# Performance work log

Measured on AMD Instinct MI355X. Metric: run time of the kernel, lower is better.

The kernel has to match this reference:

```python
import jax, jax.numpy as jnp
import numpy as np
from jax.scipy.special import logsumexp

N_ITERS = 20


def setup_inputs() -> dict:
    key = jax.random.key(0)
    k1, _ = jax.random.split(key)
    cost_matrix = jax.random.uniform(k1, (64, 1024, 1024), dtype=jnp.float32)
    epsilon = jnp.ones((1,), dtype=jnp.float32)
    return {"cost_matrix": cost_matrix, "epsilon": epsilon}


def reference(cost_matrix, epsilon):
    # log-space Sinkhorn: alternate row / column normalization in log domain
    log_alpha = -cost_matrix / epsilon  # (B, N, N)

    def step(la, _):
        la = la - logsumexp(la, axis=-1, keepdims=True)  # row normalize
        la = la - logsumexp(la, axis=-2, keepdims=True)  # col normalize
        return la, None

    log_alpha, _ = jax.lax.scan(step, log_alpha, None, length=N_ITERS)
    return jnp.exp(log_alpha)
```

## Files before the change

### kernel.cpp

```cpp
#include <hip/hip_runtime.h>
#include <hip/hip_fp16.h>


#define BATCH 64
#define N 1024
#define NITERS 20
#define ROWS_PER_BLOCK 64
#define BLOCKS_PER_BATCH (N / ROWS_PER_BLOCK)
#define THREADS 256
#define NU2 (N / 4)

union H2U { __half2 h; unsigned u; };

__device__ __forceinline__ uint2 f4_to_h4(float4 f) {
    H2U a, b;
    a.h = __float22half2_rn(make_float2(f.x, f.y));
    b.h = __float22half2_rn(make_float2(f.z, f.w));
    uint2 r; r.x = a.u; r.y = b.u;
    return r;
}

__device__ __forceinline__ float4 h4_to_f4(uint2 r) {
    H2U a, b;
    a.u = r.x; b.u = r.y;
    float2 fa = __half22float2(a.h);
    float2 fb = __half22float2(b.h);
    return make_float4(fa.x, fa.y, fb.x, fb.y);
}


__global__ __launch_bounds__(THREADS) void sk_zero(float* __restrict__ csum_all) {
    const int i = blockIdx.x * THREADS + threadIdx.x;
    csum_all[i] = 0.0f;
}

__global__ __launch_bounds__(THREADS) void sk_build(
        const float* __restrict__ C, const float* __restrict__ eps,
        uint2* __restrict__ K, float* __restrict__ u,
        float* __restrict__ csum_out) {
    __shared__ float lds[2][4][8];
    const int t = threadIdx.x;
    const int b = blockIdx.y;
    const int row0 = blockIdx.x * ROWS_PER_BLOCK;
    const int lane = t & 63, wid = t >> 6;
    const float nie = -1.0f / eps[0];

    const float4* __restrict__ Cp = (const float4*)(C + ((size_t)b * N + row0) * N) + t;
    uint2* __restrict__ Kp = K + ((size_t)b * N + row0) * NU2 + t;

    float4 colacc = make_float4(0.f, 0.f, 0.f, 0.f);
    float4 cur[8];
    #pragma unroll
    for (int r = 0; r < 8; ++r) cur[r] = Cp[r * 256];

    for (int chunk = 0; chunk < 8; ++chunk) {
        float4 nxt[8];
        if (chunk < 7) {
            #pragma unroll
            for (int r = 0; r < 8; ++r) nxt[r] = Cp[(chunk * 8 + 8 + r) * 256];
        }
        float4 k[8]; float s[8];
        #pragma unroll
        for (int r = 0; r < 8; ++r) {
            k[r].x = __expf(cur[r].x * nie);
            k[r].y = __expf(cur[r].y * nie);
            k[r].z = __expf(cur[r].z * nie);
            k[r].w = __expf(cur[r].w * nie);
            s[r] = (k[r].x + k[r].y) + (k[r].z + k[r].w);
            Kp[(chunk * 8 + r) * NU2] = f4_to_h4(k[r]);
        }
        #pragma unroll
        for (int off = 32; off; off >>= 1)
            #pragma unroll
            for (int r = 0; r < 8; ++r) s[r] += __shfl_xor(s[r], off, 64);
        const int p = chunk & 1;
        if (lane == 0) {
            #pragma unroll
            for (int r = 0; r < 8; ++r) lds[p][wid][r] = s[r];
        }
        __syncthreads();
        float ui[8];
        #pragma unroll
        for (int r = 0; r < 8; ++r)
            ui[r] = 1.0f / (((lds[p][0][r] + lds[p][1][r]) + (lds[p][2][r] + lds[p][3][r])));
        if (t < 8)
            u[b * N + row0 + chunk * 8 + t] =
                1.0f / ((lds[p][0][t] + lds[p][1][t]) + (lds[p][2][t] + lds[p][3][t]));
        #pragma unroll
        for (int r = 0; r < 8; ++r) {
            colacc.x += k[r].x * ui[r];
            colacc.y += k[r].y * ui[r];
            colacc.z += k[r].z * ui[r];
            colacc.w += k[r].w * ui[r];
        }
        #pragma unroll
        for (int r = 0; r < 8; ++r) cur[r] = nxt[r];
    }
    float* cs = csum_out + b * N + 4 * t;
    atomicAdd(cs + 0, colacc.x);
    atomicAdd(cs + 1, colacc.y);
    atomicAdd(cs + 2, colacc.z);
    atomicAdd(cs + 3, colacc.w);
}

__global__ __launch_bounds__(THREADS) void sk_iter(
        const uint2* __restrict__ K, const float* __restrict__ csum_in,
        float* __restrict__ u, float* __restrict__ csum_out) {
    __shared__ float lds[2][4][8];
    const int t = threadIdx.x;
    const int b = blockIdx.y;
    const int row0 = blockIdx.x * ROWS_PER_BLOCK;
    const int lane = t & 63, wid = t >> 6;

    const float4 ci = ((const float4*)(csum_in + b * N))[t];
    const float4 vv = make_float4(1.0f / ci.x, 1.0f / ci.y, 1.0f / ci.z, 1.0f / ci.w);
    const uint2* __restrict__ Kp = K + ((size_t)b * N + row0) * NU2 + t;

    float4 colacc = make_float4(0.f, 0.f, 0.f, 0.f);
    uint2 cur[8];
    #pragma unroll
    for (int r = 0; r < 8; ++r) cur[r] = Kp[r * NU2];

    for (int chunk = 0; chunk < 8; ++chunk) {
        uint2 nxt[8];
        if (chunk < 7) {
            #pragma unroll
            for (int r = 0; r < 8; ++r) nxt[r] = Kp[(chunk * 8 + 8 + r) * NU2];
        }
        float4 k[8]; float s[8];
        #pragma unroll
        for (int r = 0; r < 8; ++r) {
            k[r] = h4_to_f4(cur[r]);
            s[r] = (k[r].x * vv.x + k[r].y * vv.y) + (k[r].z * vv.z + k[r].w * vv.w);
        }
        #pragma unroll
        for (int off = 32; off; off >>= 1)
            #pragma unroll
            for (int r = 0; r < 8; ++r) s[r] += __shfl_xor(s[r], off, 64);
        const int p = chunk & 1;
        if (lane == 0) {
            #pragma unroll
            for (int r = 0; r < 8; ++r) lds[p][wid][r] = s[r];
        }
        __syncthreads();
        float ui[8];
        #pragma unroll
        for (int r = 0; r < 8; ++r)
            ui[r] = 1.0f / (((lds[p][0][r] + lds[p][1][r]) + (lds[p][2][r] + lds[p][3][r])));
        if (t < 8)
            u[b * N + row0 + chunk * 8 + t] =
                1.0f / ((lds[p][0][t] + lds[p][1][t]) + (lds[p][2][t] + lds[p][3][t]));
        #pragma unroll
        for (int r = 0; r < 8; ++r) {
            colacc.x += k[r].x * ui[r];
            colacc.y += k[r].y * ui[r];
            colacc.z += k[r].z * ui[r];
            colacc.w += k[r].w * ui[r];
        }
        #pragma unroll
        for (int r = 0; r < 8; ++r) cur[r] = nxt[r];
    }
    float* cs = csum_out + b * N + 4 * t;
    atomicAdd(cs + 0, colacc.x);
    atomicAdd(cs + 1, colacc.y);
    atomicAdd(cs + 2, colacc.z);
    atomicAdd(cs + 3, colacc.w);
}

__global__ __launch_bounds__(THREADS) void sk_final(
        const uint2* __restrict__ K, const float* __restrict__ u,
        const float* __restrict__ csum_last, float* __restrict__ out) {
    const int t = threadIdx.x;
    const int row = blockIdx.x;
    const int b = blockIdx.y;
    const float ui = u[b * N + row];
    const float4 ci = ((const float4*)(csum_last + b * N))[t];
    const float4 vv = make_float4(1.0f / ci.x, 1.0f / ci.y, 1.0f / ci.z, 1.0f / ci.w);
    const size_t base = (size_t)b * N + row;
    float4 k = h4_to_f4((K + base * NU2)[t]);
    float4 o;
    o.x = k.x * ui * vv.x;
    o.y = k.y * ui * vv.y;
    o.z = k.z * ui * vv.z;
    o.w = k.w * ui * vv.w;
    ((float4*)(out + base * N))[t] = o;
}


__device__ __forceinline__ float block_reduce_broadcast(float val, float* lds) {
    #pragma unroll
    for (int off = 32; off > 0; off >>= 1)
        val += __shfl_xor(val, off, 64);
    const int lane = threadIdx.x & 63;
    const int wid  = threadIdx.x >> 6;
    if (lane == 0) lds[wid] = val;
    __syncthreads();
    float total = lds[0] + lds[1] + lds[2] + lds[3];
    __syncthreads();
    return total;
}

__global__ __launch_bounds__(THREADS) void sink_init(float* __restrict__ v,
                                                     float* __restrict__ colsum) {
    const int i = blockIdx.x * THREADS + threadIdx.x;
    v[i] = 1.0f;
    colsum[i] = 0.0f;
}

__global__ __launch_bounds__(THREADS) void sink_iter(
        const float* __restrict__ C, const float* __restrict__ eps,
        const float* __restrict__ v, float* __restrict__ u,
        float* __restrict__ colsum) {
    __shared__ float lds[4];
    const int t = threadIdx.x;
    const int b = blockIdx.y;
    const int row0 = blockIdx.x * ROWS_PER_BLOCK;
    const float neg_inv_eps = -1.0f / eps[0];

    const float4 vv = ((const float4*)(v + b * N))[t];
    const float4* __restrict__ Cp = (const float4*)(C + ((size_t)b * N + row0) * N);

    float4 colacc = make_float4(0.f, 0.f, 0.f, 0.f);
    float4 cur = Cp[t];
    for (int i = 0; i < ROWS_PER_BLOCK; ++i) {
        float4 nxt = cur;
        if (i + 1 < ROWS_PER_BLOCK)
            nxt = Cp[(size_t)(i + 1) * (N / 4) + t];

        float4 k;
        k.x = __expf(cur.x * neg_inv_eps);
        k.y = __expf(cur.y * neg_inv_eps);
        k.z = __expf(cur.z * neg_inv_eps);
        k.w = __expf(cur.w * neg_inv_eps);

        float s = k.x * vv.x + k.y * vv.y + k.z * vv.z + k.w * vv.w;
        float S = block_reduce_broadcast(s, lds);
        float ui = 1.0f / S;
        if (t == 0) u[b * N + row0 + i] = ui;

        colacc.x += k.x * ui;
        colacc.y += k.y * ui;
        colacc.z += k.z * ui;
        colacc.w += k.w * ui;
        cur = nxt;
    }

    float* cs = colsum + b * N + 4 * t;
    atomicAdd(cs + 0, colacc.x);
    atomicAdd(cs + 1, colacc.y);
    atomicAdd(cs + 2, colacc.z);
    atomicAdd(cs + 3, colacc.w);
}

__global__ __launch_bounds__(THREADS) void sink_fix(float* __restrict__ v,
                                                    float* __restrict__ colsum) {
    const int i = blockIdx.x * THREADS + threadIdx.x;
    v[i] = 1.0f / colsum[i];
    colsum[i] = 0.0f;
}

__global__ __launch_bounds__(THREADS) void sink_final(
        const float* __restrict__ C, const float* __restrict__ eps,
        const float* __restrict__ u, const float* __restrict__ v,
        float* __restrict__ out) {
    const int t = threadIdx.x;
    const int row = blockIdx.x;
    const int b = blockIdx.y;
    const float neg_inv_eps = -1.0f / eps[0];
    const float ui = u[b * N + row];
    const float4 vv = ((const float4*)(v + b * N))[t];
    const size_t base = ((size_t)b * N + row) * N;
    float4 c = ((const float4*)(C + base))[t];
    float4 o;
    o.x = __expf(c.x * neg_inv_eps) * ui * vv.x;
    o.y = __expf(c.y * neg_inv_eps) * ui * vv.y;
    o.z = __expf(c.z * neg_inv_eps) * ui * vv.z;
    o.w = __expf(c.w * neg_inv_eps) * ui * vv.w;
    ((float4*)(out + base))[t] = o;
}


extern "C" void kernel_launch(void* const* d_in, const int* in_sizes, int n_in,
                              void* d_out, int out_size, void* d_ws, size_t ws_size,
                              hipStream_t stream) {
    const float* C   = (const float*)d_in[0];
    const float* eps = (const float*)d_in[1];
    float* out = (float*)d_out;

    const size_t k_bytes  = (size_t)BATCH * N * N * 2;
    const size_t uv_elems = (size_t)BATCH * N;
    const size_t needed   = k_bytes + uv_elems * 4 * (1 + NITERS);

    if (ws_size >= needed) {
        uint2* K      = (uint2*)d_ws;
        float* u      = (float*)((char*)d_ws + k_bytes);
        float* csum   = u + uv_elems;

        sk_zero<<<dim3(NITERS * uv_elems / THREADS), dim3(THREADS), 0, stream>>>(csum);
        sk_build<<<dim3(BLOCKS_PER_BATCH, BATCH), dim3(THREADS), 0, stream>>>(
            C, eps, K, u, csum);
        for (int it = 2; it <= NITERS; ++it) {
            sk_iter<<<dim3(BLOCKS_PER_BATCH, BATCH), dim3(THREADS), 0, stream>>>(
                K, csum + (size_t)(it - 2) * uv_elems, u,
                csum + (size_t)(it - 1) * uv_elems);
        }
        sk_final<<<dim3(N, BATCH), dim3(THREADS), 0, stream>>>(
            K, u, csum + (size_t)(NITERS - 1) * uv_elems, out);
    } else {
        float* u      = (float*)d_ws;
        float* v      = u + uv_elems;
        float* colsum = v + uv_elems;
        sink_init<<<dim3(BATCH * N / THREADS), dim3(THREADS), 0, stream>>>(v, colsum);
        for (int it = 0; it < NITERS; ++it) {
            sink_iter<<<dim3(BLOCKS_PER_BATCH, BATCH), dim3(THREADS), 0, stream>>>(
                C, eps, v, u, colsum);
            sink_fix<<<dim3(BATCH * N / THREADS), dim3(THREADS), 0, stream>>>(v, colsum);
        }
        sink_final<<<dim3(N, BATCH), dim3(THREADS), 0, stream>>>(C, eps, u, v, out);
    }
}
```

Measured before the change: 1.115 ms.

## Give each wavefront whole rows to drop per-chunk block barriers

The build and iteration kernels are restructured so each 64-lane wavefront owns 16 full rows, with every lane holding 16 contiguous columns loaded as 16-byte vectors. Row sums then need only a wave shuffle reduction, which removes the per-chunk LDS exchange and __syncthreads. Column partial sums from the four waves are combined once through shared memory before the global atomics. In exchange each thread keeps 16 column accumulators, which raises register use, and there is less memory-level parallelism per iteration (two 16-byte loads in flight per thread instead of eight 8-byte loads).

Measured after the change: 1.090 ms. 2.2% less time.

```diff
diff --git a/kernel.cpp b/kernel.cpp
--- a/kernel.cpp
+++ b/kernel.cpp
@@ -9,6 +9,7 @@
 #define BLOCKS_PER_BATCH (N / ROWS_PER_BLOCK)
 #define THREADS 256
 #define NU2 (N / 4)
+#define NU4 (N / 8)
 
 union H2U { __half2 h; unsigned u; };
 
@@ -28,6 +29,25 @@
     return make_float4(fa.x, fa.y, fb.x, fb.y);
 }
 
+__device__ __forceinline__ void h8_unpack(uint4 r, float* f) {
+    H2U a, b, c, d;
+    a.u = r.x; b.u = r.y; c.u = r.z; d.u = r.w;
+    float2 fa = __half22float2(a.h), fb = __half22float2(b.h);
+    float2 fc = __half22float2(c.h), fd = __half22float2(d.h);
+    f[0] = fa.x; f[1] = fa.y; f[2] = fb.x; f[3] = fb.y;
+    f[4] = fc.x; f[5] = fc.y; f[6] = fd.x; f[7] = fd.y;
+}
+
+__device__ __forceinline__ uint4 h8_pack(const float* f) {
+    H2U a, b, c, d;
+    a.h = __float22half2_rn(make_float2(f[0], f[1]));
+    b.h = __float22half2_rn(make_float2(f[2], f[3]));
+    c.h = __float22half2_rn(make_float2(f[4], f[5]));
+    d.h = __float22half2_rn(make_float2(f[6], f[7]));
+    uint4 r; r.x = a.u; r.y = b.u; r.z = c.u; r.w = d.u;
+    return r;
+}
+
 
 __global__ __launch_bounds__(THREADS) void sk_zero(float* __restrict__ csum_all) {
     const int i = blockIdx.x * THREADS + threadIdx.x;
@@ -36,135 +56,145 @@
 
 __global__ __launch_bounds__(THREADS) void sk_build(
         const float* __restrict__ C, const float* __restrict__ eps,
-        uint2* __restrict__ K, float* __restrict__ u,
+        uint4* __restrict__ K, float* __restrict__ u,
         float* __restrict__ csum_out) {
-    __shared__ float lds[2][4][8];
-    const int t = threadIdx.x;
-    const int b = blockIdx.y;
-    const int row0 = blockIdx.x * ROWS_PER_BLOCK;
-    const int lane = t & 63, wid = t >> 6;
+    __shared__ float4 smc[4][N / 4];
+    const int t = threadIdx.x;
+    const int lane = t & 63, w = t >> 6;
+    const int b = blockIdx.y;
+    const int row0 = blockIdx.x * ROWS_PER_BLOCK + w * 16;
     const float nie = -1.0f / eps[0];
 
-    const float4* __restrict__ Cp = (const float4*)(C + ((size_t)b * N + row0) * N) + t;
-    uint2* __restrict__ Kp = K + ((size_t)b * N + row0) * NU2 + t;
-
-    float4 colacc = make_float4(0.f, 0.f, 0.f, 0.f);
-    float4 cur[8];
-    #pragma unroll
-    for (int r = 0; r < 8; ++r) cur[r] = Cp[r * 256];
-
-    for (int chunk = 0; chunk < 8; ++chunk) {
-        float4 nxt[8];
-        if (chunk < 7) {
+    const float4* __restrict__ Cp =
+        (const float4*)(C + ((size_t)b * N + row0) * N) + lane * 4;
+    uint4* __restrict__ Kp = K + ((size_t)b * N + row0) * NU4 + lane * 2;
+
+    float colacc[16];
+    #pragma unroll
+    for (int q = 0; q < 16; ++q) colacc[q] = 0.0f;
+
+    float4 cur[4];
+    #pragma unroll
+    for (int q = 0; q < 4; ++q) cur[q] = Cp[q];
+
+    for (int i = 0; i < 16; ++i) {
+        float4 nxt[4];
+        if (i < 15) {
             #pragma unroll
-            for (int r = 0; r < 8; ++r) nxt[r] = Cp[(chunk * 8 + 8 + r) * 256];
-        }
-        float4 k[8]; float s[8];
-        #pragma unroll
-        for (int r = 0; r < 8; ++r) {
-            k[r].x = __expf(cur[r].x * nie);
-            k[r].y = __expf(cur[r].y * nie);
-            k[r].z = __expf(cur[r].z * nie);
-            k[r].w = __expf(cur[r].w * nie);
-            s[r] = (k[r].x + k[r].y) + (k[r].z + k[r].w);
-            Kp[(chunk * 8 + r) * NU2] = f4_to_h4(k[r]);
-        }
-        #pragma unroll
-        for (int off = 32; off; off >>= 1)
+            for (int q = 0; q < 4; ++q) nxt[q] = Cp[(i + 1) * (N / 4) + q];
+        }
+        float k[16];
+        const float* cf = (const float*)cur;
+        #pragma unroll
+        for (int q = 0; q < 16; ++q) k[q] = __expf(cf[q] * nie);
+
+        Kp[(size_t)i * NU4]     = h8_pack(k);
+        Kp[(size_t)i * NU4 + 1] = h8_pack(k + 8);
+
+        float s = (((k[0] + k[1]) + (k[2] + k[3])) + ((k[4] + k[5]) + (k[6] + k[7])))
+                + (((k[8] + k[9]) + (k[10] + k[11])) + ((k[12] + k[13]) + (k[14] + k[15])));
+        #pragma unroll
+        for (int off = 32; off; off >>= 1) s += __shfl_xor(s, off, 64);
+        const float ui = 1.0f / s;
+        if (lane == 0) u[b * N + row0 + i] = ui;
+
+        #pragma unroll
+        for (int q = 0; q < 16; ++q) colacc[q] += k[q] * ui;
+
+        if (i < 15) {
             #pragma unroll
-            for (int r = 0; r < 8; ++r) s[r] += __shfl_xor(s[r], off, 64);
-        const int p = chunk & 1;
-        if (lane == 0) {
-            #pragma unroll
-            for (int r = 0; r < 8; ++r) lds[p][wid][r] = s[r];
-        }
-        __syncthreads();
-        float ui[8];
-        #pragma unroll
-        for (int r = 0; r < 8; ++r)
-            ui[r] = 1.0f / (((lds[p][0][r] + lds[p][1][r]) + (lds[p][2][r] + lds[p][3][r])));
-        if (t < 8)
-            u[b * N + row0 + chunk * 8 + t] =
-                1.0f / ((lds[p][0][t] + lds[p][1][t]) + (lds[p][2][t] + lds[p][3][t]));
-        #pragma unroll
-        for (int r = 0; r < 8; ++r) {
-            colacc.x += k[r].x * ui[r];
-            colacc.y += k[r].y * ui[r];
-            colacc.z += k[r].z * ui[r];
-            colacc.w += k[r].w * ui[r];
-        }
-        #pragma unroll
-        for (int r = 0; r < 8; ++r) cur[r] = nxt[r];
-    }
+            for (int q = 0; q < 4; ++q) cur[q] = nxt[q];
+        }
+    }
+
+    #pragma unroll
+    for (int q = 0; q < 4; ++q)
+        smc[w][lane * 4 + q] = make_float4(colacc[4 * q], colacc[4 * q + 1],
+                                           colacc[4 * q + 2], colacc[4 * q + 3]);
+    __syncthreads();
+    float4 s0 = smc[0][t], s1 = smc[1][t], s2 = smc[2][t], s3 = smc[3][t];
+    float4 sum;
+    sum.x = (s0.x + s1.x) + (s2.x + s3.x);
+    sum.y = (s0.y + s1.y) + (s2.y + s3.y);
+    sum.z = (s0.z + s1.z) + (s2.z + s3.z);
+    sum.w = (s0.w + s1.w) + (s2.w + s3.w);
     float* cs = csum_out + b * N + 4 * t;
-    atomicAdd(cs + 0, colacc.x);
-    atomicAdd(cs + 1, colacc.y);
-    atomicAdd(cs + 2, colacc.z);
-    atomicAdd(cs + 3, colacc.w);
+    atomicAdd(cs + 0, sum.x);
+    atomicAdd(cs + 1, sum.y);
+    atomicAdd(cs + 2, sum.z);
+    atomicAdd(cs + 3, sum.w);
 }
 
 __global__ __launch_bounds__(THREADS) void sk_iter(
-        const uint2* __restrict__ K, const float* __restrict__ csum_in,
+        const uint4* __restrict__ K, const float* __restrict__ csum_in,
         float* __restrict__ u, float* __restrict__ csum_out) {
-    __shared__ float lds[2][4][8];
-    const int t = threadIdx.x;
-    const int b = blockIdx.y;
-    const int row0 = blockIdx.x * ROWS_PER_BLOCK;
-    const int lane = t & 63, wid = t >> 6;
-
-    const float4 ci = ((const float4*)(csum_in + b * N))[t];
-    const float4 vv = make_float4(1.0f / ci.x, 1.0f / ci.y, 1.0f / ci.z, 1.0f / ci.w);
-    const uint2* __restrict__ Kp = K + ((size_t)b * N + row0) * NU2 + t;
-
-    float4 colacc = make_float4(0.f, 0.f, 0.f, 0.f);
-    uint2 cur[8];
-    #pragma unroll
-    for (int r = 0; r < 8; ++r) cur[r] = Kp[r * NU2];
-
-    for (int chunk = 0; chunk < 8; ++chunk) {
-        uint2 nxt[8];
-        if (chunk < 7) {
-            #pragma unroll
-            for (int r = 0; r < 8; ++r) nxt[r] = Kp[(chunk * 8 + 8 + r) * NU2];
-        }
-        float4 k[8]; float s[8];
-        #pragma unroll
-        for (int r = 0; r < 8; ++r) {
-            k[r] = h4_to_f4(cur[r]);
-            s[r] = (k[r].x * vv.x + k[r].y * vv.y) + (k[r].z * vv.z + k[r].w * vv.w);
-        }
-        #pragma unroll
-        for (int off = 32; off; off >>= 1)
-            #pragma unroll
-            for (int r = 0; r < 8; ++r) s[r] += __shfl_xor(s[r], off, 64);
-        const int p = chunk & 1;
-        if (lane == 0) {
-            #pragma unroll
-            for (int r = 0; r < 8; ++r) lds[p][wid][r] = s[r];
-        }
-        __syncthreads();
-        float ui[8];
-        #pragma unroll
-        for (int r = 0; r < 8; ++r)
-            ui[r] = 1.0f / (((lds[p][0][r] + lds[p][1][r]) + (lds[p][2][r] + lds[p][3][r])));
-        if (t < 8)
-            u[b * N + row0 + chunk * 8 + t] =
-                1.0f / ((lds[p][0][t] + lds[p][1][t]) + (lds[p][2][t] + lds[p][3][t]));
-        #pragma unroll
-        for (int r = 0; r < 8; ++r) {
-            colacc.x += k[r].x * ui[r];
-            colacc.y += k[r].y * ui[r];
-            colacc.z += k[r].z * ui[r];
-            colacc.w += k[r].w * ui[r];
-        }
-        #pragma unroll
-        for (int r = 0; r < 8; ++r) cur[r] = nxt[r];
-    }
+    __shared__ float4 smc[4][N / 4];
+    const int t = threadIdx.x;
+    const int lane = t & 63, w = t >> 6;
+    const int b = blockIdx.y;
+    const int row0 = blockIdx.x * ROWS_PER_BLOCK + w * 16;
+
+    const float4* __restrict__ cin = (const float4*)(csum_in + b * N) + lane * 4;
+    float vv[16];
+    #pragma unroll
+    for (int q = 0; q < 4; ++q) {
+        float4 c = cin[q];
+        vv[4 * q + 0] = 1.0f / c.x;
+        vv[4 * q + 1] = 1.0f / c.y;
+        vv[4 * q + 2] = 1.0f / c.z;
+        vv[4 * q + 3] = 1.0f / c.w;
+    }
+
+    const uint4* __restrict__ Kp = K + ((size_t)b * N + row0) * NU4 + lane * 2;
+
+    float colacc[16];
+    #pragma unroll
+    for (int q = 0; q < 16; ++q) colacc[q] = 0.0f;
+
+    uint4 c0 = Kp[0], c1 = Kp[1];
+    for (int i = 0; i < 16; ++i) {
+        uint4 n0, n1;
+        if (i < 15) {
+            n0 = Kp[(size_t)(i + 1) * NU4];
+            n1 = Kp[(size_t)(i + 1) * NU4 + 1];
+        }
+        float k[16];
+        h8_unpack(c0, k);
+        h8_unpack(c1, k + 8);
+
+        float pa = (k[0] * vv[0] + k[1] * vv[1]) + (k[2] * vv[2] + k[3] * vv[3]);
+        float pb = (k[4] * vv[4] + k[5] * vv[5]) + (k[6] * vv[6] + k[7] * vv[7]);
+        float pc = (k[8] * vv[8] + k[9] * vv[9]) + (k[10] * vv[10] + k[11] * vv[11]);
+        float pd = (k[12] * vv[12] + k[13] * vv[13]) + (k[14] * vv[14] + k[15] * vv[15]);
+        float s = (pa + pb) + (pc + pd);
+
+        #pragma unroll
+        for (int off = 32; off; off >>= 1) s += __shfl_xor(s, off, 64);
+        const float ui = 1.0f / s;
+        if (lane == 0) u[b * N + row0 + i] = ui;
+
+        #pragma unroll
+        for (int q = 0; q < 16; ++q) colacc[q] += k[q] * ui;
+
+        if (i < 15) { c0 = n0; c1 = n1; }
+    }
+
+    #pragma unroll
+    for (int q = 0; q < 4; ++q)
+        smc[w][lane * 4 + q] = make_float4(colacc[4 * q], colacc[4 * q + 1],
+                                           colacc[4 * q + 2], colacc[4 * q + 3]);
+    __syncthreads();
+    float4 s0 = smc[0][t], s1 = smc[1][t], s2 = smc[2][t], s3 = smc[3][t];
+    float4 sum;
+    sum.x = (s0.x + s1.x) + (s2.x + s3.x);
+    sum.y = (s0.y + s1.y) + (s2.y + s3.y);
+    sum.z = (s0.z + s1.z) + (s2.z + s3.z);
+    sum.w = (s0.w + s1.w) + (s2.w + s3.w);
     float* cs = csum_out + b * N + 4 * t;
-    atomicAdd(cs + 0, colacc.x);
-    atomicAdd(cs + 1, colacc.y);
-    atomicAdd(cs + 2, colacc.z);
-    atomicAdd(cs + 3, colacc.w);
+    atomicAdd(cs + 0, sum.x);
+    atomicAdd(cs + 1, sum.y);
+    atomicAdd(cs + 2, sum.z);
+    atomicAdd(cs + 3, sum.w);
 }
 
 __global__ __launch_bounds__(THREADS) void sk_final(
@@ -292,7 +322,7 @@
     const size_t needed   = k_bytes + uv_elems * 4 * (1 + NITERS);
 
     if (ws_size >= needed) {
-        uint2* K      = (uint2*)d_ws;
+        uint4* K      = (uint4*)d_ws;
         float* u      = (float*)((char*)d_ws + k_bytes);
         float* csum   = u + uv_elems;
 
@@ -305,7 +335,7 @@
                 csum + (size_t)(it - 1) * uv_elems);
         }
         sk_final<<<dim3(N, BATCH), dim3(THREADS), 0, stream>>>(
-            K, u, csum + (size_t)(NITERS - 1) * uv_elems, out);
+            (const uint2*)K, u, csum + (size_t)(NITERS - 1) * uv_elems, out);
     } else {
         float* u      = (float*)d_ws;
         float* v      = u + uv_elems;
```
